# Optimization experiments

Measured on AMD Instinct MI355X. Metric: run time of the kernel, lower is better.

Reference implementation:

```python
import jax, jax.numpy as jnp
import numpy as np

N = 100000      # nodes
D = 64          # input feature dim
L0, L1 = 64, 32 # layer sizes
EP = 400000     # positive edges
EN = 400000     # negative edges
LAMB = 1.0


def _scatter_mean(feats, rows, num_nodes):
    # mean of feats grouped by destination node `rows`; empty nodes -> 0
    s = jax.ops.segment_sum(feats, rows, num_segments=num_nodes)
    c = jax.ops.segment_sum(jnp.ones((rows.shape[0],), feats.dtype), rows, num_segments=num_nodes)
    return s / jnp.maximum(c, 1.0)[:, None]


def _base_layer(x, edges, W, b):
    row, col = edges[0], edges[1]
    agg = _scatter_mean(x[col], row, x.shape[0])          # [N, D]
    return jnp.tanh(jnp.concatenate([agg, x], axis=1) @ W + b)


def _deep_layer(x1, x2, pos_edges, neg_edges, W, b):
    agg1 = _scatter_mean(x1[pos_edges[1]], pos_edges[0], x1.shape[0])
    agg2 = _scatter_mean(x2[neg_edges[1]], neg_edges[0], x2.shape[0])
    return jnp.tanh(jnp.concatenate([agg1, agg2, x1], axis=1) @ W + b)


def _xavier(key, shape):
    fan_in, fan_out = shape[0], shape[1]
    lim = np.sqrt(6.0 / (fan_in + fan_out)).astype(np.float32)
    return jax.random.uniform(key, shape, jnp.float32, -lim, lim)


def setup_inputs() -> dict:
    key = jax.random.key(0)
    ks = jax.random.split(key, 12)
    X = jax.random.normal(ks[0], (N, D), jnp.float32)
    W_pos0 = _xavier(ks[1], (2 * D, L0)); b_pos0 = jnp.zeros((L0,), jnp.float32)
    W_neg0 = _xavier(ks[2], (2 * D, L0)); b_neg0 = jnp.zeros((L0,), jnp.float32)
    W_pos1 = _xavier(ks[3], (3 * L0, L1)); b_pos1 = jnp.zeros((L1,), jnp.float32)
    W_neg1 = _xavier(ks[4], (3 * L0, L1)); b_neg1 = jnp.zeros((L1,), jnp.float32)
    W_reg = _xavier(ks[5], (4 * L1, 2))
    positive_edges = jax.random.randint(ks[6], (2, EP), 0, N)
    negative_edges = jax.random.randint(ks[7], (2, EN), 0, N)
    target = jax.random.randint(ks[8], (EP + EN,), 0, 2)
    pos_samples = jax.random.randint(ks[9], (EP,), 0, N)
    neg_samples = jax.random.randint(ks[10], (EN,), 0, N)
    return {"X": X, "W_pos0": W_pos0, "b_pos0": b_pos0, "W_neg0": W_neg0,
            "b_neg0": b_neg0, "W_pos1": W_pos1, "b_pos1": b_pos1,
            "W_neg1": W_neg1, "b_neg1": b_neg1, "W_reg": W_reg,
            "positive_edges": positive_edges, "negative_edges": negative_edges,
            "target": target, "pos_samples": pos_samples, "neg_samples": neg_samples}


def _triplet_loss(z, edges, samples):
    zi = z[edges[0]]
    zj = z[edges[1]]
    zk = z[samples]
    norm_ij = jnp.sum((zi - zj) ** 2, axis=1)
    norm_ik = jnp.sum((zj - zk) ** 2, axis=1)
    return jnp.mean(jnp.maximum(norm_ij - norm_ik, 0.0)), zi, zj


def reference(X, W_pos0, b_pos0, W_neg0, b_neg0, W_pos1, b_pos1,
              W_neg1, b_neg1, W_reg, positive_edges, negative_edges,
              target, pos_samples, neg_samples):
    h_pos = _base_layer(X, positive_edges, W_pos0, b_pos0)
    h_neg = _base_layer(X, negative_edges, W_neg0, b_neg0)
    h_pos2 = _deep_layer(h_pos, h_neg, positive_edges, negative_edges, W_pos1, b_pos1)
    h_neg2 = _deep_layer(h_neg, h_pos, positive_edges, negative_edges, W_neg1, b_neg1)
    z = jnp.concatenate([h_pos2, h_neg2], axis=1)  # [N, 2*L1]

    loss_pos, pzi, pzj = _triplet_loss(z, positive_edges, pos_samples)
    loss_neg, nzi, nzj = _triplet_loss(z, negative_edges, neg_samples)

    feats = jnp.concatenate([
        jnp.concatenate([pzi, pzj], axis=1),
        jnp.concatenate([nzi, nzj], axis=1)], axis=0)       # [EP+EN, 4*L1]
    logp = jax.nn.log_softmax(feats @ W_reg, axis=1)
    regress = -jnp.mean(jnp.take_along_axis(logp, target[:, None], axis=1))
    loss = regress + LAMB * (loss_pos + loss_neg)
    return (loss, z)
```

## Files before the change

### kernel.cpp

```cpp
#include <hip/hip_runtime.h>
#include <cstdint>

#define N_NODES 100000
#define EP_N 400000
#define EN_N 400000
#define NODE_BLOCKS ((N_NODES + 63) / 64)
#define SCHUNK 512
#define SBLK ((N_NODES + SCHUNK - 1) / SCHUNK)

#define BSTR 264
#define DSTR 392

#define XB_BLKS ((((N_NODES + 1) * 16) + 255) / 256)
#define WP_BLKS 112
#define CNT_BLKS (((EP_N + EN_N) + 255) / 256)
#define EI_BLKS CNT_BLKS

#define ACC_OFF 0
#define I_CNTP 16
#define I_CNTN (I_CNTP + N_NODES)
#define I_CURP (I_CNTN + N_NODES)
#define I_CURN (I_CURP + N_NODES)
#define I_OFFP (I_CURN + N_NODES)
#define I_OFFN (I_OFFP + N_NODES + 1)
#define I_CSRP (((I_OFFN + N_NODES + 1) + 3) & ~3)
#define CSR_SZ (EP_N + 4 * N_NODES)
#define I_CSRN (I_CSRP + CSR_SZ)
#define I_PART (I_CSRN + CSR_SZ)
#define I_EIDX (((I_PART + 2 * SBLK) + 3) & ~3)
#define F_XB (((I_EIDX + 4 * (EP_N + EN_N)) + 15) & ~15)
#define F_HB (F_XB + 32 * (N_NODES + 1))
#define F_PNU (F_HB + 64 * (N_NODES + 1))
#define F_PNV (F_PNU + 4 * N_NODES)
#define F_ZQ (F_PNV + 4 * N_NODES)
#define F_WT (((F_ZQ + 16 * N_NODES) + 15) & ~15)

typedef __attribute__((ext_vector_type(8))) short sh8;
typedef __attribute__((ext_vector_type(4))) float f32x4;

__device__ inline float bf2f(unsigned short u) {
    return __uint_as_float((unsigned)u << 16);
}
__device__ inline unsigned short f2bf(float v) {
    unsigned u = __float_as_uint(v);
    return (unsigned short)((u + 0x7FFFu + ((u >> 16) & 1u)) >> 16);
}
__device__ inline float lo_bf(unsigned u) { return __uint_as_float(u << 16); }
__device__ inline float hi_bf(unsigned u) { return __uint_as_float(u & 0xFFFF0000u); }

__device__ inline float dot4f8(unsigned a, unsigned b) {
    float s = __builtin_amdgcn_cvt_f32_fp8(a, 0) * __builtin_amdgcn_cvt_f32_fp8(b, 0);
    s = fmaf(__builtin_amdgcn_cvt_f32_fp8(a, 1), __builtin_amdgcn_cvt_f32_fp8(b, 1), s);
    s = fmaf(__builtin_amdgcn_cvt_f32_fp8(a, 2), __builtin_amdgcn_cvt_f32_fp8(b, 2), s);
    s = fmaf(__builtin_amdgcn_cvt_f32_fp8(a, 3), __builtin_amdgcn_cvt_f32_fp8(b, 3), s);
    return s;
}

__global__ void prep_kernel(const float* __restrict__ X, unsigned short* __restrict__ xb,
                            const float* __restrict__ W0p, const float* __restrict__ W0n,
                            const float* __restrict__ W1p, const float* __restrict__ W1n,
                            unsigned short* __restrict__ wt,
                            const int* __restrict__ pe, const int* __restrict__ ne,
                            const int* __restrict__ ps, const int* __restrict__ ns,
                            const int* __restrict__ tgt,
                            int* cp, int* cn, int4* __restrict__ eidx) {
    int b = blockIdx.x;
    if (b < XB_BLKS) {
        int i = b * 256 + threadIdx.x;
        if (i < (N_NODES + 1) * 16) {
            ushort4 o = {0, 0, 0, 0};
            if (i < N_NODES * 16) {
                float4 v = ((const float4*)X)[i];
                o.x = f2bf(v.x); o.y = f2bf(v.y); o.z = f2bf(v.z); o.w = f2bf(v.w);
            }
            ((ushort4*)xb)[i] = o;
        }
    } else if (b < XB_BLKS + WP_BLKS) {
        int i = (b - XB_BLKS) * 256 + threadIdx.x;
        if (i < 8192) {
            int n = i >> 7, k = i & 127;
            wt[i] = f2bf(W0p[k * 64 + n]);
        } else if (i < 16384) {
            int j = i - 8192; int n = j >> 7, k = j & 127;
            wt[i] = f2bf(W0n[k * 64 + n]);
        } else if (i < 22528) {
            int j = i - 16384; int n = j / 192, k = j - n * 192;
            wt[i] = f2bf(W1p[k * 32 + n]);
        } else if (i < 28672) {
            int j = i - 22528; int n = j / 192, k = j - n * 192;
            wt[i] = f2bf(W1n[k * 32 + n]);
        }
    } else if (b < XB_BLKS + WP_BLKS + CNT_BLKS) {
        int i = (b - XB_BLKS - WP_BLKS) * 256 + threadIdx.x;
        if (i < EP_N) {
            atomicAdd(&cp[pe[i]], 1);
        } else if (i < EP_N + EN_N) {
            atomicAdd(&cn[ne[i - EP_N]], 1);
        }
    } else {
        int e = (b - XB_BLKS - WP_BLKS - CNT_BLKS) * 256 + threadIdx.x;
        if (e < EP_N) {
            int4 q = {pe[e], pe[EP_N + e], ps[e], tgt[e]};
            eidx[e] = q;
        } else if (e < EP_N + EN_N) {
            int e2 = e - EP_N;
            int4 q = {ne[e2], ne[EN_N + e2], ns[e2], tgt[e]};
            eidx[e] = q;
        }
    }
}

__global__ __launch_bounds__(512) void scan_p1(const int* __restrict__ cntP,
                                               const int* __restrict__ cntN,
                                               int* part) {
    int l = blockIdx.x < SBLK ? 0 : 1;
    int blk = blockIdx.x - l * SBLK;
    const int* cnt = l == 0 ? cntP : cntN;
    int idx = blk * SCHUNK + threadIdx.x;
    int v = idx < N_NODES ? (cnt[idx] + 3) & ~3 : 0;
    __shared__ int tmp[512];
    tmp[threadIdx.x] = v;
    __syncthreads();
    for (int d = 256; d > 0; d >>= 1) {
        if (threadIdx.x < d) tmp[threadIdx.x] += tmp[threadIdx.x + d];
        __syncthreads();
    }
    if (threadIdx.x == 0) part[l * SBLK + blk] = tmp[0];
}

__global__ __launch_bounds__(512) void scan_p2(int* part) {
    int t = threadIdx.x;
    int l = t >> 8, idx = t & 255;
    int v = idx < SBLK ? part[l * SBLK + idx] : 0;
    __shared__ int tmp[512];
    int sb = l << 8;
    tmp[sb + idx] = v;
    __syncthreads();
    for (int d = 1; d < 256; d <<= 1) {
        int x = (idx >= d) ? tmp[sb + idx - d] : 0;
        __syncthreads();
        tmp[sb + idx] += x;
        __syncthreads();
    }
    if (idx < SBLK) part[l * SBLK + idx] = tmp[sb + idx] - v;
}

__global__ __launch_bounds__(512) void scan_p3(const int* __restrict__ cntP,
                                               const int* __restrict__ cntN,
                                               const int* __restrict__ part,
                                               int* offP, int* offN,
                                               int* csrP, int* csrN) {
    int l = blockIdx.x < SBLK ? 0 : 1;
    int blk = blockIdx.x - l * SBLK;
    const int* cnt = l == 0 ? cntP : cntN;
    int* off = l == 0 ? offP : offN;
    int* csr = l == 0 ? csrP : csrN;
    int base = part[l * SBLK + blk];
    int t = threadIdx.x;
    int gidx = blk * SCHUNK + t;
    int c = gidx < N_NODES ? cnt[gidx] : 0;
    int cpad = (c + 3) & ~3;
    __shared__ int tmp[512];
    tmp[t] = cpad;
    __syncthreads();
    for (int d = 1; d < 512; d <<= 1) {
        int x = (t >= d) ? tmp[t - d] : 0;
        __syncthreads();
        tmp[t] += x;
        __syncthreads();
    }
    int incl = tmp[t];
    if (gidx < N_NODES) {
        int o = base + incl - cpad;
        off[gidx] = o;
        for (int p = c; p < cpad; ++p) csr[o + p] = N_NODES;
    }
    if (gidx == N_NODES - 1) off[N_NODES] = base + incl;
}

__global__ void fill_kernel(const int* __restrict__ pe, const int* __restrict__ ne,
                            const int* __restrict__ offP, const int* __restrict__ offN,
                            int* curP, int* curN, int* csrP, int* csrN) {
    int e = blockIdx.x * 256 + threadIdx.x;
    if (e < EP_N) {
        int row = pe[e], col = pe[EP_N + e];
        int slot = atomicAdd(&curP[row], 1);
        csrP[offP[row] + slot] = col;
    } else if (e < EP_N + EN_N) {
        int e2 = e - EP_N;
        int row = ne[e2], col = ne[EN_N + e2];
        int slot = atomicAdd(&curN[row], 1);
        csrN[offN[row] + slot] = col;
    }
}

__device__ inline void gmb2(const unsigned short* __restrict__ src,
                            const int* __restrict__ csrP, int pP, int enP, int cP,
                            const int* __restrict__ csrN, int pN, int enN, int cN,
                            int lane, float& mP, float& mN) {
    float a0 = 0.f, a1 = 0.f, a2 = 0.f, a3 = 0.f;
    float b0 = 0.f, b1 = 0.f, b2 = 0.f, b3 = 0.f;
    while (pP < enP && pN < enN) {
        int4 ca = *(const int4*)(csrP + pP);
        int4 cb = *(const int4*)(csrN + pN);
        a0 += bf2f(src[ca.x * 64 + lane]);
        a1 += bf2f(src[ca.y * 64 + lane]);
        a2 += bf2f(src[ca.z * 64 + lane]);
        a3 += bf2f(src[ca.w * 64 + lane]);
        b0 += bf2f(src[cb.x * 64 + lane]);
        b1 += bf2f(src[cb.y * 64 + lane]);
        b2 += bf2f(src[cb.z * 64 + lane]);
        b3 += bf2f(src[cb.w * 64 + lane]);
        pP += 4; pN += 4;
    }
    for (; pP < enP; pP += 4) {
        int4 ca = *(const int4*)(csrP + pP);
        a0 += bf2f(src[ca.x * 64 + lane]);
        a1 += bf2f(src[ca.y * 64 + lane]);
        a2 += bf2f(src[ca.z * 64 + lane]);
        a3 += bf2f(src[ca.w * 64 + lane]);
    }
    for (; pN < enN; pN += 4) {
        int4 cb = *(const int4*)(csrN + pN);
        b0 += bf2f(src[cb.x * 64 + lane]);
        b1 += bf2f(src[cb.y * 64 + lane]);
        b2 += bf2f(src[cb.z * 64 + lane]);
        b3 += bf2f(src[cb.w * 64 + lane]);
    }
    mP = ((a0 + a1) + (a2 + a3)) / fmaxf((float)cP, 1.f);
    mN = ((b0 + b1) + (b2 + b3)) / fmaxf((float)cN, 1.f);
}

__device__ inline void gd2(const unsigned* __restrict__ hb32,
                           const int* __restrict__ csrP, int pP, int enP, int cP,
                           const int* __restrict__ csrN, int pN, int enN, int cN,
                           int lane,
                           float& gPp, float& gPn, float& gNp, float& gNn) {
    float ap0 = 0.f, ap1 = 0.f, ap2 = 0.f, ap3 = 0.f;
    float an0 = 0.f, an1 = 0.f, an2 = 0.f, an3 = 0.f;
    float bp0 = 0.f, bp1 = 0.f, bp2 = 0.f, bp3 = 0.f;
    float bn0 = 0.f, bn1 = 0.f, bn2 = 0.f, bn3 = 0.f;
    while (pP < enP && pN < enN) {
        int4 ca = *(const int4*)(csrP + pP);
        int4 cb = *(const int4*)(csrN + pN);
        unsigned va0 = hb32[ca.x * 64 + lane];
        unsigned va1 = hb32[ca.y * 64 + lane];
        unsigned va2 = hb32[ca.z * 64 + lane];
        unsigned va3 = hb32[ca.w * 64 + lane];
        unsigned vb0 = hb32[cb.x * 64 + lane];
        unsigned vb1 = hb32[cb.y * 64 + lane];
        unsigned vb2 = hb32[cb.z * 64 + lane];
        unsigned vb3 = hb32[cb.w * 64 + lane];
        ap0 += lo_bf(va0); an0 += hi_bf(va0);
        ap1 += lo_bf(va1); an1 += hi_bf(va1);
        ap2 += lo_bf(va2); an2 += hi_bf(va2);
        ap3 += lo_bf(va3); an3 += hi_bf(va3);
        bp0 += lo_bf(vb0); bn0 += hi_bf(vb0);
        bp1 += lo_bf(vb1); bn1 += hi_bf(vb1);
        bp2 += lo_bf(vb2); bn2 += hi_bf(vb2);
        bp3 += lo_bf(vb3); bn3 += hi_bf(vb3);
        pP += 4; pN += 4;
    }
    for (; pP < enP; pP += 4) {
        int4 ca = *(const int4*)(csrP + pP);
        unsigned va0 = hb32[ca.x * 64 + lane];
        unsigned va1 = hb32[ca.y * 64 + lane];
        unsigned va2 = hb32[ca.z * 64 + lane];
        unsigned va3 = hb32[ca.w * 64 + lane];
        ap0 += lo_bf(va0); an0 += hi_bf(va0);
        ap1 += lo_bf(va1); an1 += hi_bf(va1);
        ap2 += lo_bf(va2); an2 += hi_bf(va2);
        ap3 += lo_bf(va3); an3 += hi_bf(va3);
    }
    for (; pN < enN; pN += 4) {
        int4 cb = *(const int4*)(csrN + pN);
        unsigned vb0 = hb32[cb.x * 64 + lane];
        unsigned vb1 = hb32[cb.y * 64 + lane];
        unsigned vb2 = hb32[cb.z * 64 + lane];
        unsigned vb3 = hb32[cb.w * 64 + lane];
        bp0 += lo_bf(vb0); bn0 += hi_bf(vb0);
        bp1 += lo_bf(vb1); bn1 += hi_bf(vb1);
        bp2 += lo_bf(vb2); bn2 += hi_bf(vb2);
        bp3 += lo_bf(vb3); bn3 += hi_bf(vb3);
    }
    float rP = 1.f / fmaxf((float)cP, 1.f), rN = 1.f / fmaxf((float)cN, 1.f);
    gPp = ((ap0 + ap1) + (ap2 + ap3)) * rP;
    gPn = ((an0 + an1) + (an2 + an3)) * rP;
    gNp = ((bp0 + bp1) + (bp2 + bp3)) * rN;
    gNn = ((bn0 + bn1) + (bn2 + bn3)) * rN;
}

__global__ __launch_bounds__(512) void base_both(
    const unsigned short* __restrict__ xb,
    const int* __restrict__ offP, const int* __restrict__ csrP,
    const int* __restrict__ offN, const int* __restrict__ csrN,
    const int* __restrict__ cntP, const int* __restrict__ cntN,
    const unsigned short* __restrict__ wt0,
    const float* __restrict__ bp0, const float* __restrict__ bn0,
    unsigned short* __restrict__ hboth) {
    __shared__ unsigned short lds[64 * BSTR];
    int tid = threadIdx.x, lane = tid & 63, w = tid >> 6;
    int base = blockIdx.x * 64;
    if (blockIdx.x == 0 && tid < 64) ((unsigned*)hboth)[N_NODES * 64 + tid] = 0u;
    for (int r = w * 8; r < w * 8 + 8; ++r) {
        int node = base + r;
        float gP = 0.f, gN = 0.f;
        unsigned short sx = 0;
        if (node < N_NODES) {
            gmb2(xb, csrP, offP[node], offP[node + 1], cntP[node],
                 csrN, offN[node], offN[node + 1], cntN[node], lane, gP, gN);
            sx = xb[node * 64 + lane];
        }
        unsigned short* rp = &lds[r * BSTR];
        rp[lane] = f2bf(gP);
        rp[64 + lane] = sx;
        rp[128 + lane] = f2bf(gN);
        rp[192 + lane] = sx;
    }
    __syncthreads();
    int wu = __builtin_amdgcn_readfirstlane(w);
    int mt = wu >> 1, half = wu & 1;
    int l15 = lane & 15, kq = lane >> 4;
    const unsigned short* wbase = wt0 + half * 8192;
    f32x4 acc[4];
#pragma unroll
    for (int nt = 0; nt < 4; ++nt) acc[nt] = (f32x4){0.f, 0.f, 0.f, 0.f};
    const unsigned short* arow = &lds[(mt * 16 + l15) * BSTR + half * 128 + kq * 8];
#pragma unroll
    for (int ks = 0; ks < 4; ++ks) {
        sh8 a = *(const sh8*)(arow + ks * 32);
#pragma unroll
        for (int nt = 0; nt < 4; ++nt) {
            sh8 bf = *(const sh8*)(wbase + (nt * 16 + l15) * 128 + ks * 32 + kq * 8);
            acc[nt] = __builtin_amdgcn_mfma_f32_16x16x32_bf16(a, bf, acc[nt], 0, 0, 0);
        }
    }
    __syncthreads();
    float* ht = (float*)lds;
    const float* bias = half ? bn0 : bp0;
#pragma unroll
    for (int nt = 0; nt < 4; ++nt) {
        int col = nt * 16 + l15;
        float bb = bias[col];
#pragma unroll
        for (int r = 0; r < 4; ++r) {
            int row = mt * 16 + kq * 4 + r;
            ht[row * 130 + half * 64 + col] = tanhf(acc[nt][r] + bb);
        }
    }
    __syncthreads();
    unsigned* hb32 = (unsigned*)hboth;
    for (int i = tid; i < 64 * 64; i += 512) {
        int rr = i >> 6, c = i & 63;
        int node = base + rr;
        if (node < N_NODES) {
            unsigned lo = f2bf(ht[rr * 130 + c]);
            unsigned hi = f2bf(ht[rr * 130 + 64 + c]);
            hb32[node * 64 + c] = lo | (hi << 16);
        }
    }
}

__global__ __launch_bounds__(512) void deep_both(
    const unsigned short* __restrict__ hb,
    const int* __restrict__ offP, const int* __restrict__ csrP,
    const int* __restrict__ offN, const int* __restrict__ csrN,
    const int* __restrict__ cntP, const int* __restrict__ cntN,
    const unsigned short* __restrict__ wt1,
    const float* __restrict__ bp1, const float* __restrict__ bn1,
    const float* __restrict__ Wreg, float* __restrict__ z,
    unsigned char* __restrict__ zq, float4* __restrict__ pnu,
    float4* __restrict__ pnv) {
    __shared__ unsigned short lds[64 * DSTR];
    int tid = threadIdx.x, lane = tid & 63, w = tid >> 6;
    int base = blockIdx.x * 64;
    const unsigned* hb32 = (const unsigned*)hb;
    for (int r = w * 8; r < w * 8 + 8; ++r) {
        int node = base + r;
        float gPp = 0.f, gPn = 0.f, gNp = 0.f, gNn = 0.f, sp = 0.f, sn = 0.f;
        if (node < N_NODES) {
            gd2(hb32, csrP, offP[node], offP[node + 1], cntP[node],
                csrN, offN[node], offN[node + 1], cntN[node], lane,
                gPp, gPn, gNp, gNn);
            unsigned self = hb32[node * 64 + lane];
            sp = lo_bf(self);
            sn = hi_bf(self);
        }
        unsigned short* rp = &lds[r * DSTR];
        rp[lane] = f2bf(gPp);
        rp[64 + lane] = f2bf(gNn);
        rp[128 + lane] = f2bf(sp);
        rp[192 + lane] = f2bf(gPn);
        rp[256 + lane] = f2bf(gNp);
        rp[320 + lane] = f2bf(sn);
    }
    __syncthreads();
    int wu = __builtin_amdgcn_readfirstlane(w);
    int mt = wu >> 1, half = wu & 1;
    int l15 = lane & 15, kq = lane >> 4;
    const unsigned short* wbase = wt1 + half * 6144;
    f32x4 acc[2];
    acc[0] = (f32x4){0.f, 0.f, 0.f, 0.f};
    acc[1] = (f32x4){0.f, 0.f, 0.f, 0.f};
    const unsigned short* arow = &lds[(mt * 16 + l15) * DSTR + half * 192 + kq * 8];
#pragma unroll
    for (int ks = 0; ks < 6; ++ks) {
        sh8 a = *(const sh8*)(arow + ks * 32);
#pragma unroll
        for (int nt = 0; nt < 2; ++nt) {
            sh8 bf = *(const sh8*)(wbase + (nt * 16 + l15) * 192 + ks * 32 + kq * 8);
            acc[nt] = __builtin_amdgcn_mfma_f32_16x16x32_bf16(a, bf, acc[nt], 0, 0, 0);
        }
    }
    __syncthreads();
    float* ot = (float*)lds;
    const float* bias = half ? bn1 : bp1;
#pragma unroll
    for (int nt = 0; nt < 2; ++nt) {
        int col = nt * 16 + l15;
        float bb = bias[col];
#pragma unroll
        for (int r = 0; r < 4; ++r) {
            int row = mt * 16 + kq * 4 + r;
            ot[row * 65 + half * 32 + col] = tanhf(acc[nt][r] + bb);
        }
    }
    __syncthreads();
    for (int r = w * 8; r < w * 8 + 8; ++r) {
        int node = base + r;
        if (node >= N_NODES) break;
        float v = ot[r * 65 + lane];
        z[node * 64 + lane] = v;
        int pq = __builtin_amdgcn_cvt_pk_fp8_f32(v, v, 0, false);
        zq[node * 64 + lane] = (unsigned char)(pq & 0xFF);
        float vq = __builtin_amdgcn_cvt_f32_fp8(pq, 0);
        float u0 = vq * Wreg[lane * 2 + 0];
        float u1 = vq * Wreg[lane * 2 + 1];
        float v0 = vq * Wreg[128 + lane * 2 + 0];
        float v1 = vq * Wreg[128 + lane * 2 + 1];
        float s = vq * vq;
#pragma unroll
        for (int off = 32; off; off >>= 1) {
            u0 += __shfl_xor(u0, off);
            u1 += __shfl_xor(u1, off);
            v0 += __shfl_xor(v0, off);
            v1 += __shfl_xor(v1, off);
            s += __shfl_xor(s, off);
        }
        if (lane == 0) {
            float4 su = {u0, u1, s, 0.f};
            float4 sv = {v0, v1, s, 0.f};
            pnu[node] = su;
            pnv[node] = sv;
        }
    }
}

__global__ __launch_bounds__(256) void loss6_kernel(
    const unsigned char* __restrict__ zq, const float4* __restrict__ pnu,
    const float4* __restrict__ pnv, const int4* __restrict__ eidx, float* acc) {
    int tid = threadIdx.x;
    int lane = tid & 63;
    int g = lane >> 2, sub = lane & 3;
    int wid = (blockIdx.x * 256 + tid) >> 6;
    int nw = (gridDim.x * 256) >> 6;
    float s_p = 0.f, s_n = 0.f, s_r = 0.f;
    const float q = 0.25f;
    for (int eb = wid * 32; eb < EP_N + EN_N; eb += nw * 32) {
        int eA = eb + g, eB = eb + 16 + g;
        bool vA = eA < EP_N + EN_N, vB = eB < EP_N + EN_N;
        bool pA = eA < EP_N, pB = eB < EP_N;
        int4 qA = eidx[vA ? eA : 0];
        int4 qB = eidx[vB ? eB : 0];
        uint4 ziA = *(const uint4*)(zq + ((long long)qA.x << 6) + (sub << 4));
        uint4 zjA = *(const uint4*)(zq + ((long long)qA.y << 6) + (sub << 4));
        uint4 zkA = *(const uint4*)(zq + ((long long)qA.z << 6) + (sub << 4));
        uint4 ziB = *(const uint4*)(zq + ((long long)qB.x << 6) + (sub << 4));
        uint4 zjB = *(const uint4*)(zq + ((long long)qB.y << 6) + (sub << 4));
        uint4 zkB = *(const uint4*)(zq + ((long long)qB.z << 6) + (sub << 4));
        float4 uA = pnu[qA.x];
        float4 wA = pnv[qA.y];
        float skA = pnu[qA.z].z;
        float4 uB = pnu[qB.x];
        float4 wB = pnv[qB.y];
        float skB = pnu[qB.z].z;
        float d1A = dot4f8(ziA.x, zjA.x) + dot4f8(ziA.y, zjA.y) +
                    dot4f8(ziA.z, zjA.z) + dot4f8(ziA.w, zjA.w);
        float d2A = dot4f8(zjA.x, zkA.x) + dot4f8(zjA.y, zkA.y) +
                    dot4f8(zjA.z, zkA.z) + dot4f8(zjA.w, zkA.w);
        float d1B = dot4f8(ziB.x, zjB.x) + dot4f8(ziB.y, zjB.y) +
                    dot4f8(ziB.z, zjB.z) + dot4f8(ziB.w, zjB.w);
        float d2B = dot4f8(zjB.x, zkB.x) + dot4f8(zjB.y, zkB.y) +
                    dot4f8(zjB.z, zkB.z) + dot4f8(zjB.w, zkB.w);
#pragma unroll
        for (int off = 1; off < 4; off <<= 1) {
            d1A += __shfl_xor(d1A, off);
            d2A += __shfl_xor(d2A, off);
            d1B += __shfl_xor(d1B, off);
            d2B += __shfl_xor(d2B, off);
        }
        if (vA) {
            float nij = uA.z + wA.z - 2.f * d1A;
            float nik = wA.z + skA - 2.f * d2A;
            float tri = fmaxf(nij - nik, 0.f);
            float l0 = uA.x + wA.x, l1 = uA.y + wA.y;
            float m = fmaxf(l0, l1);
            float lse = m + logf(expf(l0 - m) + expf(l1 - m));
            s_r += (lse - (qA.w ? l1 : l0)) * q;
            if (pA) s_p += tri * q; else s_n += tri * q;
        }
        if (vB) {
            float nij = uB.z + wB.z - 2.f * d1B;
            float nik = wB.z + skB - 2.f * d2B;
            float tri = fmaxf(nij - nik, 0.f);
            float l0 = uB.x + wB.x, l1 = uB.y + wB.y;
            float m = fmaxf(l0, l1);
            float lse = m + logf(expf(l0 - m) + expf(l1 - m));
            s_r += (lse - (qB.w ? l1 : l0)) * q;
            if (pB) s_p += tri * q; else s_n += tri * q;
        }
    }
#pragma unroll
    for (int off = 32; off; off >>= 1) {
        s_p += __shfl_xor(s_p, off);
        s_n += __shfl_xor(s_n, off);
        s_r += __shfl_xor(s_r, off);
    }
    __shared__ float red[3][4];
    int w = tid >> 6;
    if (lane == 0) {
        red[0][w] = s_p; red[1][w] = s_n; red[2][w] = s_r;
    }
    __syncthreads();
    if (tid == 0) {
        atomicAdd(&acc[0], red[0][0] + red[0][1] + red[0][2] + red[0][3]);
        atomicAdd(&acc[1], red[1][0] + red[1][1] + red[1][2] + red[1][3]);
        atomicAdd(&acc[2], red[2][0] + red[2][1] + red[2][2] + red[2][3]);
    }
}

__global__ void finalize_kernel(const float* __restrict__ acc, float* out) {
    out[0] = acc[2] / (float)(EP_N + EN_N) +
             1.0f * (acc[0] / (float)EP_N + acc[1] / (float)EN_N);
}

extern "C" void kernel_launch(void* const* d_in, const int* in_sizes, int n_in,
                              void* d_out, int out_size, void* d_ws, size_t ws_size,
                              hipStream_t stream) {
    const float* X = (const float*)d_in[0];
    const float* W_pos0 = (const float*)d_in[1];
    const float* b_pos0 = (const float*)d_in[2];
    const float* W_neg0 = (const float*)d_in[3];
    const float* b_neg0 = (const float*)d_in[4];
    const float* W_pos1 = (const float*)d_in[5];
    const float* b_pos1 = (const float*)d_in[6];
    const float* W_neg1 = (const float*)d_in[7];
    const float* b_neg1 = (const float*)d_in[8];
    const float* W_reg = (const float*)d_in[9];
    const int* pe = (const int*)d_in[10];
    const int* ne = (const int*)d_in[11];
    const int* target = (const int*)d_in[12];
    const int* ps = (const int*)d_in[13];
    const int* ns = (const int*)d_in[14];
    float* out = (float*)d_out;
    float* ws = (float*)d_ws;
    int* wsi = (int*)d_ws;

    float* acc = ws + ACC_OFF;
    int* cntP = wsi + I_CNTP;
    int* cntN = wsi + I_CNTN;
    int* curP = wsi + I_CURP;
    int* curN = wsi + I_CURN;
    int* offP = wsi + I_OFFP;
    int* offN = wsi + I_OFFN;
    int* csrP = wsi + I_CSRP;
    int* csrN = wsi + I_CSRN;
    int* part = wsi + I_PART;
    int4* eidx = (int4*)(wsi + I_EIDX);
    unsigned short* xb = (unsigned short*)(ws + F_XB);
    unsigned short* hboth = (unsigned short*)(ws + F_HB);
    float4* pnu = (float4*)(ws + F_PNU);
    float4* pnv = (float4*)(ws + F_PNV);
    unsigned char* zq = (unsigned char*)(ws + F_ZQ);
    unsigned short* wt = (unsigned short*)(ws + F_WT);
    float* z = out + 1;

    hipMemsetAsync(ws, 0, (size_t)(16 + 4 * N_NODES) * sizeof(float), stream);

    prep_kernel<<<XB_BLKS + WP_BLKS + CNT_BLKS + EI_BLKS, 256, 0, stream>>>(
        X, xb, W_pos0, W_neg0, W_pos1, W_neg1, wt, pe, ne, ps, ns, target,
        cntP, cntN, eidx);
    scan_p1<<<2 * SBLK, 512, 0, stream>>>(cntP, cntN, part);
    scan_p2<<<1, 512, 0, stream>>>(part);
    scan_p3<<<2 * SBLK, 512, 0, stream>>>(cntP, cntN, part, offP, offN, csrP, csrN);
    fill_kernel<<<(EP_N + EN_N + 255) / 256, 256, 0, stream>>>(pe, ne, offP, offN,
                                                               curP, curN, csrP, csrN);

    base_both<<<NODE_BLOCKS, 512, 0, stream>>>(xb, offP, csrP, offN, csrN, cntP, cntN,
                                               wt, b_pos0, b_neg0, hboth);
    deep_both<<<NODE_BLOCKS, 512, 0, stream>>>(hboth, offP, csrP, offN, csrN, cntP, cntN,
                                               wt + 16384, b_pos1, b_neg1,
                                               W_reg, z, zq, pnu, pnv);

    loss6_kernel<<<2048, 256, 0, stream>>>(zq, pnu, pnv, eidx, acc);
    finalize_kernel<<<1, 1, 0, stream>>>(acc, out);
}
```

Baseline: 366.5 us.

## Split wavefront halves across neighbor slots and use wider feature loads in gathers

The neighbor gathers now give each half-wavefront a different pair of neighbors from every group of four. Each lane loads two packed bf16 features (32-bit in base, 64-bit in deep), and the partial sums of the two halves are combined with a cross-half shuffle. This is meant to cut the number of memory requests per neighbor and raise the bytes moved per load. The deep kernel also drops to 32 nodes per block, with each wave computing a single MFMA tile, which doubles the grid for more parallelism. The bounds checks were removed on the assumption that N divides evenly by 32, and the CSR is padded to multiples of four.

```diff
diff --git a/kernel.cpp b/kernel.cpp
--- a/kernel.cpp
+++ b/kernel.cpp
@@ -5,6 +5,7 @@
 #define EP_N 400000
 #define EN_N 400000
 #define NODE_BLOCKS ((N_NODES + 63) / 64)
+#define DEEP_BLOCKS (N_NODES / 32)
 #define SCHUNK 512
 #define SBLK ((N_NODES + SCHUNK - 1) / SCHUNK)
 
@@ -194,100 +195,112 @@
     }
 }
 
-__device__ inline void gmb2(const unsigned short* __restrict__ src,
-                            const int* __restrict__ csrP, int pP, int enP, int cP,
-                            const int* __restrict__ csrN, int pN, int enN, int cN,
-                            int lane, float& mP, float& mN) {
-    float a0 = 0.f, a1 = 0.f, a2 = 0.f, a3 = 0.f;
-    float b0 = 0.f, b1 = 0.f, b2 = 0.f, b3 = 0.f;
+__device__ inline void gmb2w(const unsigned* __restrict__ xb32,
+                             const int* __restrict__ csrP, int pP, int enP, int cP,
+                             const int* __restrict__ csrN, int pN, int enN, int cN,
+                             int hf, int l5,
+                             float& gP0, float& gP1, float& gN0, float& gN1) {
+    float a0 = 0.f, a1 = 0.f, b0 = 0.f, b1 = 0.f;
     while (pP < enP && pN < enN) {
         int4 ca = *(const int4*)(csrP + pP);
         int4 cb = *(const int4*)(csrN + pN);
-        a0 += bf2f(src[ca.x * 64 + lane]);
-        a1 += bf2f(src[ca.y * 64 + lane]);
-        a2 += bf2f(src[ca.z * 64 + lane]);
-        a3 += bf2f(src[ca.w * 64 + lane]);
-        b0 += bf2f(src[cb.x * 64 + lane]);
-        b1 += bf2f(src[cb.y * 64 + lane]);
-        b2 += bf2f(src[cb.z * 64 + lane]);
-        b3 += bf2f(src[cb.w * 64 + lane]);
+        int cA0 = hf ? ca.y : ca.x;
+        int cA1 = hf ? ca.w : ca.z;
+        int cB0 = hf ? cb.y : cb.x;
+        int cB1 = hf ? cb.w : cb.z;
+        unsigned va0 = xb32[cA0 * 32 + l5];
+        unsigned va1 = xb32[cA1 * 32 + l5];
+        unsigned vb0 = xb32[cB0 * 32 + l5];
+        unsigned vb1 = xb32[cB1 * 32 + l5];
+        a0 += lo_bf(va0) + lo_bf(va1);
+        a1 += hi_bf(va0) + hi_bf(va1);
+        b0 += lo_bf(vb0) + lo_bf(vb1);
+        b1 += hi_bf(vb0) + hi_bf(vb1);
         pP += 4; pN += 4;
     }
     for (; pP < enP; pP += 4) {
         int4 ca = *(const int4*)(csrP + pP);
-        a0 += bf2f(src[ca.x * 64 + lane]);
-        a1 += bf2f(src[ca.y * 64 + lane]);
-        a2 += bf2f(src[ca.z * 64 + lane]);
-        a3 += bf2f(src[ca.w * 64 + lane]);
+        int cA0 = hf ? ca.y : ca.x;
+        int cA1 = hf ? ca.w : ca.z;
+        unsigned va0 = xb32[cA0 * 32 + l5];
+        unsigned va1 = xb32[cA1 * 32 + l5];
+        a0 += lo_bf(va0) + lo_bf(va1);
+        a1 += hi_bf(va0) + hi_bf(va1);
     }
     for (; pN < enN; pN += 4) {
         int4 cb = *(const int4*)(csrN + pN);
-        b0 += bf2f(src[cb.x * 64 + lane]);
-        b1 += bf2f(src[cb.y * 64 + lane]);
-        b2 += bf2f(src[cb.z * 64 + lane]);
-        b3 += bf2f(src[cb.w * 64 + lane]);
-    }
-    mP = ((a0 + a1) + (a2 + a3)) / fmaxf((float)cP, 1.f);
-    mN = ((b0 + b1) + (b2 + b3)) / fmaxf((float)cN, 1.f);
-}
-
-__device__ inline void gd2(const unsigned* __restrict__ hb32,
-                           const int* __restrict__ csrP, int pP, int enP, int cP,
-                           const int* __restrict__ csrN, int pN, int enN, int cN,
-                           int lane,
-                           float& gPp, float& gPn, float& gNp, float& gNn) {
-    float ap0 = 0.f, ap1 = 0.f, ap2 = 0.f, ap3 = 0.f;
-    float an0 = 0.f, an1 = 0.f, an2 = 0.f, an3 = 0.f;
-    float bp0 = 0.f, bp1 = 0.f, bp2 = 0.f, bp3 = 0.f;
-    float bn0 = 0.f, bn1 = 0.f, bn2 = 0.f, bn3 = 0.f;
+        int cB0 = hf ? cb.y : cb.x;
+        int cB1 = hf ? cb.w : cb.z;
+        unsigned vb0 = xb32[cB0 * 32 + l5];
+        unsigned vb1 = xb32[cB1 * 32 + l5];
+        b0 += lo_bf(vb0) + lo_bf(vb1);
+        b1 += hi_bf(vb0) + hi_bf(vb1);
+    }
+    a0 += __shfl_xor(a0, 32); a1 += __shfl_xor(a1, 32);
+    b0 += __shfl_xor(b0, 32); b1 += __shfl_xor(b1, 32);
+    float rP = 1.f / fmaxf((float)cP, 1.f), rN = 1.f / fmaxf((float)cN, 1.f);
+    gP0 = a0 * rP; gP1 = a1 * rP;
+    gN0 = b0 * rN; gN1 = b1 * rN;
+}
+
+__device__ inline void gd2w(const unsigned* __restrict__ hb32,
+                            const int* __restrict__ csrP, int pP, int enP, int cP,
+                            const int* __restrict__ csrN, int pN, int enN, int cN,
+                            int hf, int l5,
+                            float& gPp0, float& gPp1, float& gPn0, float& gPn1,
+                            float& gNp0, float& gNp1, float& gNn0, float& gNn1) {
+    float ap0 = 0.f, ap1 = 0.f, an0 = 0.f, an1 = 0.f;
+    float bp0 = 0.f, bp1 = 0.f, bn0 = 0.f, bn1 = 0.f;
     while (pP < enP && pN < enN) {
         int4 ca = *(const int4*)(csrP + pP);
         int4 cb = *(const int4*)(csrN + pN);
-        unsigned va0 = hb32[ca.x * 64 + lane];
-        unsigned va1 = hb32[ca.y * 64 + lane];
-        unsigned va2 = hb32[ca.z * 64 + lane];
-        unsigned va3 = hb32[ca.w * 64 + lane];
-        unsigned vb0 = hb32[cb.x * 64 + lane];
-        unsigned vb1 = hb32[cb.y * 64 + lane];
-        unsigned vb2 = hb32[cb.z * 64 + lane];
-        unsigned vb3 = hb32[cb.w * 64 + lane];
-        ap0 += lo_bf(va0); an0 += hi_bf(va0);
-        ap1 += lo_bf(va1); an1 += hi_bf(va1);
-        ap2 += lo_bf(va2); an2 += hi_bf(va2);
-        ap3 += lo_bf(va3); an3 += hi_bf(va3);
-        bp0 += lo_bf(vb0); bn0 += hi_bf(vb0);
-        bp1 += lo_bf(vb1); bn1 += hi_bf(vb1);
-        bp2 += lo_bf(vb2); bn2 += hi_bf(vb2);
-        bp3 += lo_bf(vb3); bn3 += hi_bf(vb3);
+        int cA0 = hf ? ca.y : ca.x;
+        int cA1 = hf ? ca.w : ca.z;
+        int cB0 = hf ? cb.y : cb.x;
+        int cB1 = hf ? cb.w : cb.z;
+        uint2 va0 = *(const uint2*)(hb32 + cA0 * 64 + l5 * 2);
+        uint2 va1 = *(const uint2*)(hb32 + cA1 * 64 + l5 * 2);
+        uint2 vb0 = *(const uint2*)(hb32 + cB0 * 64 + l5 * 2);
+        uint2 vb1 = *(const uint2*)(hb32 + cB1 * 64 + l5 * 2);
+        ap0 += lo_bf(va0.x) + lo_bf(va1.x);
+        an0 += hi_bf(va0.x) + hi_bf(va1.x);
+        ap1 += lo_bf(va0.y) + lo_bf(va1.y);
+        an1 += hi_bf(va0.y) + hi_bf(va1.y);
+        bp0 += lo_bf(vb0.x) + lo_bf(vb1.x);
+        bn0 += hi_bf(vb0.x) + hi_bf(vb1.x);
+        bp1 += lo_bf(vb0.y) + lo_bf(vb1.y);
+        bn1 += hi_bf(vb0.y) + hi_bf(vb1.y);
         pP += 4; pN += 4;
     }
     for (; pP < enP; pP += 4) {
         int4 ca = *(const int4*)(csrP + pP);
-        unsigned va0 = hb32[ca.x * 64 + lane];
-        unsigned va1 = hb32[ca.y * 64 + lane];
-        unsigned va2 = hb32[ca.z * 64 + lane];
-        unsigned va3 = hb32[ca.w * 64 + lane];
-        ap0 += lo_bf(va0); an0 += hi_bf(va0);
-        ap1 += lo_bf(va1); an1 += hi_bf(va1);
-        ap2 += lo_bf(va2); an2 += hi_bf(va2);
-        ap3 += lo_bf(va3); an3 += hi_bf(va3);
+        int cA0 = hf ? ca.y : ca.x;
+        int cA1 = hf ? ca.w : ca.z;
+        uint2 va0 = *(const uint2*)(hb32 + cA0 * 64 + l5 * 2);
+        uint2 va1 = *(const uint2*)(hb32 + cA1 * 64 + l5 * 2);
+        ap0 += lo_bf(va0.x) + lo_bf(va1.x);
+        an0 += hi_bf(va0.x) + hi_bf(va1.x);
+        ap1 += lo_bf(va0.y) + lo_bf(va1.y);
+        an1 += hi_bf(va0.y) + hi_bf(va1.y);
     }
     for (; pN < enN; pN += 4) {
         int4 cb = *(const int4*)(csrN + pN);
-        unsigned vb0 = hb32[cb.x * 64 + lane];
-        unsigned vb1 = hb32[cb.y * 64 + lane];
-        unsigned vb2 = hb32[cb.z * 64 + lane];
-        unsigned vb3 = hb32[cb.w * 64 + lane];
-        bp0 += lo_bf(vb0); bn0 += hi_bf(vb0);
-        bp1 += lo_bf(vb1); bn1 += hi_bf(vb1);
-        bp2 += lo_bf(vb2); bn2 += hi_bf(vb2);
-        bp3 += lo_bf(vb3); bn3 += hi_bf(vb3);
-    }
+        int cB0 = hf ? cb.y : cb.x;
+        int cB1 = hf ? cb.w : cb.z;
+        uint2 vb0 = *(const uint2*)(hb32 + cB0 * 64 + l5 * 2);
+        uint2 vb1 = *(const uint2*)(hb32 + cB1 * 64 + l5 * 2);
+        bp0 += lo_bf(vb0.x) + lo_bf(vb1.x);
+        bn0 += hi_bf(vb0.x) + hi_bf(vb1.x);
+        bp1 += lo_bf(vb0.y) + lo_bf(vb1.y);
+        bn1 += hi_bf(vb0.y) + hi_bf(vb1.y);
+    }
+    ap0 += __shfl_xor(ap0, 32); ap1 += __shfl_xor(ap1, 32);
+    an0 += __shfl_xor(an0, 32); an1 += __shfl_xor(an1, 32);
+    bp0 += __shfl_xor(bp0, 32); bp1 += __shfl_xor(bp1, 32);
+    bn0 += __shfl_xor(bn0, 32); bn1 += __shfl_xor(bn1, 32);
     float rP = 1.f / fmaxf((float)cP, 1.f), rN = 1.f / fmaxf((float)cN, 1.f);
-    gPp = ((ap0 + ap1) + (ap2 + ap3)) * rP;
-    gPn = ((an0 + an1) + (an2 + an3)) * rP;
-    gNp = ((bp0 + bp1) + (bp2 + bp3)) * rN;
-    gNn = ((bn0 + bn1) + (bn2 + bn3)) * rN;
+    gPp0 = ap0 * rP; gPp1 = ap1 * rP; gPn0 = an0 * rP; gPn1 = an1 * rP;
+    gNp0 = bp0 * rN; gNp1 = bp1 * rN; gNn0 = bn0 * rN; gNn1 = bn1 * rN;
 }
 
 __global__ __launch_bounds__(512) void base_both(
@@ -300,22 +313,28 @@
     unsigned short* __restrict__ hboth) {
     __shared__ unsigned short lds[64 * BSTR];
     int tid = threadIdx.x, lane = tid & 63, w = tid >> 6;
+    int hf = lane >> 5, l5 = lane & 31;
     int base = blockIdx.x * 64;
+    const unsigned* xb32 = (const unsigned*)xb;
     if (blockIdx.x == 0 && tid < 64) ((unsigned*)hboth)[N_NODES * 64 + tid] = 0u;
     for (int r = w * 8; r < w * 8 + 8; ++r) {
         int node = base + r;
-        float gP = 0.f, gN = 0.f;
-        unsigned short sx = 0;
+        float gP0 = 0.f, gP1 = 0.f, gN0 = 0.f, gN1 = 0.f;
+        unsigned sxv = 0;
         if (node < N_NODES) {
-            gmb2(xb, csrP, offP[node], offP[node + 1], cntP[node],
-                 csrN, offN[node], offN[node + 1], cntN[node], lane, gP, gN);
-            sx = xb[node * 64 + lane];
-        }
-        unsigned short* rp = &lds[r * BSTR];
-        rp[lane] = f2bf(gP);
-        rp[64 + lane] = sx;
-        rp[128 + lane] = f2bf(gN);
-        rp[192 + lane] = sx;
+            gmb2w(xb32, csrP, offP[node], offP[node + 1], cntP[node],
+                  csrN, offN[node], offN[node + 1], cntN[node], hf, l5,
+                  gP0, gP1, gN0, gN1);
+            sxv = xb32[node * 32 + l5];
+        }
+        unsigned* rp32 = (unsigned*)&lds[r * BSTR];
+        if (hf == 0) {
+            rp32[l5] = (unsigned)f2bf(gP0) | ((unsigned)f2bf(gP1) << 16);
+            rp32[32 + l5] = sxv;
+        } else {
+            rp32[64 + l5] = (unsigned)f2bf(gN0) | ((unsigned)f2bf(gN1) << 16);
+            rp32[96 + l5] = sxv;
+        }
     }
     __syncthreads();
     int wu = __builtin_amdgcn_readfirstlane(w);
@@ -371,64 +390,57 @@
     const float* __restrict__ Wreg, float* __restrict__ z,
     unsigned char* __restrict__ zq, float4* __restrict__ pnu,
     float4* __restrict__ pnv) {
-    __shared__ unsigned short lds[64 * DSTR];
+    __shared__ unsigned short lds[32 * DSTR];
     int tid = threadIdx.x, lane = tid & 63, w = tid >> 6;
-    int base = blockIdx.x * 64;
+    int hf = lane >> 5, l5 = lane & 31;
+    int base = blockIdx.x * 32;
     const unsigned* hb32 = (const unsigned*)hb;
-    for (int r = w * 8; r < w * 8 + 8; ++r) {
+    for (int r = w * 4; r < w * 4 + 4; ++r) {
         int node = base + r;
-        float gPp = 0.f, gPn = 0.f, gNp = 0.f, gNn = 0.f, sp = 0.f, sn = 0.f;
-        if (node < N_NODES) {
-            gd2(hb32, csrP, offP[node], offP[node + 1], cntP[node],
-                csrN, offN[node], offN[node + 1], cntN[node], lane,
-                gPp, gPn, gNp, gNn);
-            unsigned self = hb32[node * 64 + lane];
-            sp = lo_bf(self);
-            sn = hi_bf(self);
-        }
-        unsigned short* rp = &lds[r * DSTR];
-        rp[lane] = f2bf(gPp);
-        rp[64 + lane] = f2bf(gNn);
-        rp[128 + lane] = f2bf(sp);
-        rp[192 + lane] = f2bf(gPn);
-        rp[256 + lane] = f2bf(gNp);
-        rp[320 + lane] = f2bf(sn);
+        float gPp0, gPp1, gPn0, gPn1, gNp0, gNp1, gNn0, gNn1;
+        gd2w(hb32, csrP, offP[node], offP[node + 1], cntP[node],
+             csrN, offN[node], offN[node + 1], cntN[node], hf, l5,
+             gPp0, gPp1, gPn0, gPn1, gNp0, gNp1, gNn0, gNn1);
+        uint2 sv = *(const uint2*)(hb32 + node * 64 + l5 * 2);
+        unsigned* rp32 = (unsigned*)&lds[r * DSTR];
+        if (hf == 0) {
+            rp32[l5] = (unsigned)f2bf(gPp0) | ((unsigned)f2bf(gPp1) << 16);
+            rp32[32 + l5] = (unsigned)f2bf(gNn0) | ((unsigned)f2bf(gNn1) << 16);
+            rp32[64 + l5] = (sv.x & 0xFFFFu) | ((sv.y & 0xFFFFu) << 16);
+        } else {
+            rp32[96 + l5] = (unsigned)f2bf(gPn0) | ((unsigned)f2bf(gPn1) << 16);
+            rp32[128 + l5] = (unsigned)f2bf(gNp0) | ((unsigned)f2bf(gNp1) << 16);
+            rp32[160 + l5] = (sv.x >> 16) | (sv.y & 0xFFFF0000u);
+        }
     }
     __syncthreads();
     int wu = __builtin_amdgcn_readfirstlane(w);
-    int mt = wu >> 1, half = wu & 1;
+    int mt = wu >> 2, half = (wu >> 1) & 1, nt = wu & 1;
     int l15 = lane & 15, kq = lane >> 4;
     const unsigned short* wbase = wt1 + half * 6144;
-    f32x4 acc[2];
-    acc[0] = (f32x4){0.f, 0.f, 0.f, 0.f};
-    acc[1] = (f32x4){0.f, 0.f, 0.f, 0.f};
+    f32x4 acc = (f32x4){0.f, 0.f, 0.f, 0.f};
     const unsigned short* arow = &lds[(mt * 16 + l15) * DSTR + half * 192 + kq * 8];
 #pragma unroll
     for (int ks = 0; ks < 6; ++ks) {
         sh8 a = *(const sh8*)(arow + ks * 32);
-#pragma unroll
-        for (int nt = 0; nt < 2; ++nt) {
-            sh8 bf = *(const sh8*)(wbase + (nt * 16 + l15) * 192 + ks * 32 + kq * 8);
-            acc[nt] = __builtin_amdgcn_mfma_f32_16x16x32_bf16(a, bf, acc[nt], 0, 0, 0);
-        }
+        sh8 bf = *(const sh8*)(wbase + (nt * 16 + l15) * 192 + ks * 32 + kq * 8);
+        acc = __builtin_amdgcn_mfma_f32_16x16x32_bf16(a, bf, acc, 0, 0, 0);
     }
     __syncthreads();
     float* ot = (float*)lds;
-    const float* bias = half ? bn1 : bp1;
-#pragma unroll
-    for (int nt = 0; nt < 2; ++nt) {
+    {
+        const float* bias = half ? bn1 : bp1;
         int col = nt * 16 + l15;
         float bb = bias[col];
 #pragma unroll
         for (int r = 0; r < 4; ++r) {
             int row = mt * 16 + kq * 4 + r;
-            ot[row * 65 + half * 32 + col] = tanhf(acc[nt][r] + bb);
-        }
-    }
-    __syncthreads();
-    for (int r = w * 8; r < w * 8 + 8; ++r) {
+            ot[row * 65 + half * 32 + col] = tanhf(acc[r] + bb);
+        }
+    }
+    __syncthreads();
+    for (int r = w * 4; r < w * 4 + 4; ++r) {
         int node = base + r;
-        if (node >= N_NODES) break;
         float v = ot[r * 65 + lane];
         z[node * 64 + lane] = v;
         int pq = __builtin_amdgcn_cvt_pk_fp8_f32(v, v, 0, false);
@@ -449,9 +461,9 @@
         }
         if (lane == 0) {
             float4 su = {u0, u1, s, 0.f};
-            float4 sv = {v0, v1, s, 0.f};
+            float4 sv2 = {v0, v1, s, 0.f};
             pnu[node] = su;
-            pnv[node] = sv;
+            pnv[node] = sv2;
         }
     }
 }
@@ -598,7 +610,7 @@
 
     base_both<<<NODE_BLOCKS, 512, 0, stream>>>(xb, offP, csrP, offN, csrN, cntP, cntN,
                                                wt, b_pos0, b_neg0, hboth);
-    deep_both<<<NODE_BLOCKS, 512, 0, stream>>>(hboth, offP, csrP, offN, csrN, cntP, cntN,
+    deep_both<<<DEEP_BLOCKS, 512, 0, stream>>>(hboth, offP, csrP, offN, csrN, cntP, cntN,
                                                wt + 16384, b_pos1, b_neg1,
                                                W_reg, z, zq, pnu, pnv);
 
```

New measurement: 353.0 us. -3.7%, faster.
